# Optimization experiments

Measured on AMD Instinct MI355X. Metric: run time of the kernel, lower is better.

Reference implementation:

```python
import jax, jax.numpy as jnp
import numpy as np
import math

B, T, C, H = 2, 2048, 1024, 16
D = C // H  # head dim 64

def setup_inputs() -> dict:
    key = jax.random.key(0)
    ks = jax.random.split(key, 3)
    scale = 0.02
    return {
        "x": jax.random.normal(ks[0], (B, T, C), dtype=jnp.float32),
        "W_attn": jax.random.normal(ks[1], (C, 3 * C), dtype=jnp.float32) * scale,
        "b_attn": jnp.zeros((3 * C,), dtype=jnp.float32),
        "W_proj": jax.random.normal(ks[2], (C, C), dtype=jnp.float32) * scale,
        "b_proj": jnp.zeros((C,), dtype=jnp.float32),
    }

def reference(x, W_attn, b_attn, W_proj, b_proj):
    Bb, Tt, Cc = x.shape
    qkv = x @ W_attn + b_attn                       # [B,T,3C]
    q, k, v = jnp.split(qkv, 3, axis=-1)
    # [B,T,C] -> [B,H,T,D]
    def heads(t):
        return t.reshape(Bb, Tt, H, D).transpose(0, 2, 1, 3)
    q, k, v = heads(q), heads(k), heads(v)
    scores = jnp.einsum('bhqd,bhkd->bhqk', q, k) * (1.0 / math.sqrt(D))
    causal = jnp.tril(jnp.ones((Tt, Tt), dtype=bool))
    scores = jnp.where(causal, scores, -jnp.inf)
    attn = jax.nn.softmax(scores, axis=-1)
    out = jnp.einsum('bhqk,bhkd->bhqd', attn, v)    # [B,H,T,D]
    out = out.transpose(0, 2, 1, 3).reshape(Bb, Tt, Cc)
    return out @ W_proj + b_proj
```

## Files before the change

### kernel.cpp

```cpp
#include <hip/hip_runtime.h>

typedef unsigned short u16;
typedef unsigned int u32;
typedef float f32x4 __attribute__((ext_vector_type(4)));
typedef float f32x16 __attribute__((ext_vector_type(16)));
typedef unsigned int u32x4 __attribute__((ext_vector_type(4)));
typedef unsigned int u32x2 __attribute__((ext_vector_type(2)));
typedef unsigned short u16x8 __attribute__((ext_vector_type(8)));
typedef unsigned short u16x4 __attribute__((ext_vector_type(4)));

#define DEV static __device__ __forceinline__

constexpr int BB = 2, TT = 2048, CC = 1024, HH = 16, DD = 64;
constexpr int MDIM = BB * TT;

DEV u16 f2bf(float f) {
  unsigned int u = __builtin_bit_cast(unsigned int, f);
  u += 0x7fffu + ((u >> 16) & 1u);
  return (u16)(u >> 16);
}
DEV float bf2f(u16 h) {
  unsigned int u = ((unsigned int)h) << 16;
  return __builtin_bit_cast(float, u);
}
DEV void async16(const void* g, void* l) {
  __builtin_amdgcn_global_load_lds(
      (const __attribute__((address_space(1))) unsigned int*)g,
      (__attribute__((address_space(3))) unsigned int*)l, 16, 0, 0);
}
DEV void mfma16(f32x4& acc, u32x4 a, u32x4 b) {
  asm volatile("v_mfma_f32_16x16x32_bf16 %0, %1, %2, %0"
               : "+v"(acc)
               : "v"(a), "v"(b));
}
DEV void mfma32(f32x16& acc, u32x4 a, u32x4 b) {
  asm volatile("v_mfma_f32_32x32x16_bf16 %0, %1, %2, %0"
               : "+v"(acc)
               : "v"(a), "v"(b));
}
DEV u32 cvtpk(float lo, float hi) {
  u32 r;
  asm("v_cvt_pk_bf16_f32 %0, %1, %2" : "=v"(r) : "v"(lo), "v"(hi));
  return r;
}
DEV void pswap(u32& a, u32& b) {
#if __has_builtin(__builtin_amdgcn_permlane32_swap)
  u32x2 r = __builtin_amdgcn_permlane32_swap(a, b, false, false);
  a = r.x;
  b = r.y;
#else
  asm volatile("v_permlane32_swap_b32 %0, %1" : "+v"(a), "+v"(b));
#endif
}
DEV float exp2g(float x) {
#if __has_builtin(__builtin_amdgcn_exp2f)
  return __builtin_amdgcn_exp2f(x);
#else
  return exp2f(x);
#endif
}

__global__ void cvt_f32_bf16(const float* __restrict__ in, u16* __restrict__ out, int n) {
  const int i = (blockIdx.x * blockDim.x + threadIdx.x) * 4;
  if (i < n) {
    f32x4 v = *(const f32x4*)(in + i);
    u16x4 o;
#pragma unroll
    for (int j = 0; j < 4; ++j) o[j] = f2bf(v[j]);
    *(u16x4*)(out + i) = o;
  }
}

__global__ void transpose_both(const float* __restrict__ Wa, const float* __restrict__ Wp,
                               u16* __restrict__ Wa_t, u16* __restrict__ Wp_t) {
  __shared__ float tile[32][33];
  int bx = blockIdx.x;
  const float* in;
  u16* out;
  int Cc;
  if (bx < 96) { in = Wa; out = Wa_t; Cc = 3072; }
  else { bx -= 96; in = Wp; out = Wp_t; Cc = 1024; }
  const int R = 1024;
  const int x0 = bx * 32, y0 = blockIdx.y * 32;
  const int tx = threadIdx.x, ty = threadIdx.y;
  tile[ty][tx] = in[(size_t)(y0 + ty) * Cc + (x0 + tx)];
  __syncthreads();
  out[(size_t)(x0 + ty) * R + (y0 + tx)] = f2bf(tile[tx][ty]);
}

template <int MODE>
__global__ __launch_bounds__(256) void gemm_bf16(
    const u16* __restrict__ A, const u16* __restrict__ Bt,
    const float* __restrict__ bias, float* __restrict__ outF,
    u16* __restrict__ qw, u16* __restrict__ kw, u16* __restrict__ vw,
    int M, int N, int K) {
  __shared__ alignas(16) u16 Sh[2][128 * 64];
  u16* Asp = Sh[0];
  u16* Bsp = Sh[1];
  const int tid = threadIdx.x;
  const int lane = tid & 63, w = tid >> 6;
  const int g = lane >> 4, c16 = lane & 15;
  const int wm = (w >> 1) * 64, wn = (w & 1) * 64;

  const int wgid = blockIdx.y * gridDim.x + blockIdx.x;
  const int xcd = wgid & 7, pi = wgid >> 3;
  int bxs, bys;
  if (MODE == 1) {
    bxs = 12 * (xcd & 1) + pi % 12;
    bys = 8 * (xcd >> 1) + pi / 12;
  } else {
    bxs = pi & 7;
    bys = 4 * xcd + (pi >> 3);
  }
  const int brow = bys * 128, bcol = bxs * 128;

  const int lrow = lane >> 3;
  const int scol = ((lane & 7) ^ lrow) << 4;
  const int rswz = (c16 & 7) << 4;

  f32x4 acc[4][4];
#pragma unroll
  for (int m = 0; m < 4; ++m)
#pragma unroll
    for (int n = 0; n < 4; ++n) acc[m][n] = f32x4{0.f, 0.f, 0.f, 0.f};

  const size_t ldb = (size_t)K * 2;
  const char* Abase = (const char*)A + (size_t)brow * ldb;
  const char* Bbase = (const char*)Bt + (size_t)bcol * ldb;

  for (int kt = 0; kt < K; kt += 64) {
    __syncthreads();
#pragma unroll
    for (int i = 0; i < 4; ++i) {
      const int chunk = i * 4 + w;
      const int row = chunk * 8 + lrow;
      async16(Abase + (size_t)row * ldb + (size_t)kt * 2 + scol, (char*)Asp + chunk * 1024);
      async16(Bbase + (size_t)row * ldb + (size_t)kt * 2 + scol, (char*)Bsp + chunk * 1024);
    }
    __syncthreads();
#pragma unroll
    for (int kc = 0; kc < 2; ++kc) {
      const int cb = (kc * 64 + g * 16) ^ rswz;
      u32x4 af[4], bf8[4];
#pragma unroll
      for (int m = 0; m < 4; ++m)
        af[m] = *(const u32x4*)((const char*)Asp + (wm + m * 16 + c16) * 128 + cb);
#pragma unroll
      for (int n = 0; n < 4; ++n)
        bf8[n] = *(const u32x4*)((const char*)Bsp + (wn + n * 16 + c16) * 128 + cb);
#pragma unroll
      for (int m = 0; m < 4; ++m)
#pragma unroll
        for (int n = 0; n < 4; ++n) mfma16(acc[m][n], af[m], bf8[n]);
    }
  }

  if (MODE == 0) {
    float* Ef = (float*)&Sh[0][0];
#pragma unroll
    for (int pass = 0; pass < 2; ++pass) {
      __syncthreads();
      if ((wm >> 6) == pass) {
#pragma unroll
        for (int n = 0; n < 4; ++n) {
          const float bv = bias[bcol + wn + n * 16 + c16];
#pragma unroll
          for (int m = 0; m < 4; ++m)
#pragma unroll
            for (int r = 0; r < 4; ++r)
              Ef[(m * 16 + g * 4 + r) * 128 + wn + n * 16 + c16] = acc[m][n][r] + bv;
        }
      }
      __syncthreads();
#pragma unroll
      for (int i = 0; i < 8; ++i) {
        const int chunk = tid + i * 256;
        const int row = chunk >> 5;
        const int c4 = (chunk & 31) * 4;
        f32x4 v4 = *(const f32x4*)&Ef[row * 128 + c4];
        *(f32x4*)&outF[(size_t)(brow + pass * 64 + row) * N + bcol + c4] = v4;
      }
    }
  } else {
    u16* E = &Sh[0][0];
    const int which = bcol >> 10;
    __syncthreads();
    if (which < 2) {
#pragma unroll
      for (int n = 0; n < 4; ++n) {
        const float bv = bias[bcol + wn + n * 16 + c16];
#pragma unroll
        for (int m = 0; m < 4; ++m)
#pragma unroll
          for (int r = 0; r < 4; ++r)
            E[(wm + m * 16 + g * 4 + r) * 128 + wn + n * 16 + c16] =
                f2bf(acc[m][n][r] + bv);
      }
    } else {
#pragma unroll
      for (int n = 0; n < 4; ++n) {
        const float bv = bias[bcol + wn + n * 16 + c16];
#pragma unroll
        for (int m = 0; m < 4; ++m) {
          u16x4 t4;
#pragma unroll
          for (int r = 0; r < 4; ++r) t4[r] = f2bf(acc[m][n][r] + bv);
          *(u16x4*)&E[(wn + n * 16 + c16) * 128 + wm + m * 16 + g * 4] = t4;
        }
      }
    }
    __syncthreads();
#pragma unroll
    for (int i = 0; i < 8; ++i) {
      const int chunk = tid + i * 256;
      if (which < 2) {
        const int row = chunk >> 4;
        const int cc8 = (chunk & 15) * 8;
        const int colg = bcol + cc8;
        const int c = colg & 1023, h = c >> 6, d = c & 63;
        const int rowg = brow + row, b = rowg >> 11, t = rowg & (TT - 1);
        u16x8 v8 = *(const u16x8*)&E[row * 128 + cc8];
        u16* dst = (which == 0 ? qw : kw) + ((size_t)(b * HH + h) * TT + t) * DD + d;
        *(u16x8*)dst = v8;
      } else {
        const int drow = chunk >> 4;
        const int t8 = (chunk & 15) * 8;
        const int colg = bcol + drow;
        const int c = colg & 1023, h = c >> 6, d = c & 63;
        const int rowg = brow + t8, b = rowg >> 11, t = rowg & (TT - 1);
        u16x8 v8 = *(const u16x8*)&E[drow * 128 + t8];
        u16* dst = vw + ((size_t)(b * HH + h) * DD + d) * TT + t;
        *(u16x8*)dst = v8;
      }
    }
  }
}

__global__ __launch_bounds__(256) void attn_fwd(
    const u16* __restrict__ qw, const u16* __restrict__ kw,
    const u16* __restrict__ vw, u16* __restrict__ ao) {
  extern __shared__ u16 smem[];
  const int tid = threadIdx.x;
  const int lane = tid & 63, w = tid >> 6;
  const int ql = lane & 31, half = lane >> 5;
  const int bh = blockIdx.y;
  const int qb = ((bh >> 4) & 1) ? (15 - blockIdx.x) : blockIdx.x;
  const int q0w = qb * 128 + w * 32;
  const int qg = q0w + ql;
  const int lrow = lane >> 3;
  const int scol = ((lane & 7) ^ lrow) << 4;
  const int rswz = (ql & 7) << 4;

  u32x4 qf[4];
  {
    const u16* qrow = qw + ((size_t)bh * TT + qg) * DD;
    const float qs = 0.125f * 1.44269504f;
#pragma unroll
    for (int dwin = 0; dwin < 4; ++dwin) {
      u16x8 u = *(const u16x8*)(qrow + dwin * 16 + half * 8);
      u16x8 s;
#pragma unroll
      for (int j = 0; j < 8; ++j) s[j] = f2bf(bf2f(u[j]) * qs);
      qf[dwin] = __builtin_bit_cast(u32x4, s);
    }
  }

  f32x16 o0, o1;
#pragma unroll
  for (int i = 0; i < 16; ++i) { o0[i] = 0.f; o1[i] = 0.f; }
  float l_run = 0.f;

  const char* kbase = (const char*)kw + ((size_t)bh * TT) * 128;
  const char* vbase = (const char*)vw + ((size_t)bh * DD) * (TT * 2);

  const int nt = 2 * qb + 2;

  auto kptr = [&](int b) { return (char*)(smem + b * 4096); };
  auto vptr = [&](int b) { return (char*)(smem + 16384 + b * 4096); };

  auto STAGE = [&](int kt_) {
    if (kt_ >= nt) return;
    const int buf = kt_ & 3;
    const int t0_ = kt_ * 64;
#pragma unroll
    for (int i_ = 0; i_ < 2; ++i_) {
      const int chunk = w * 2 + i_;
      const int row = chunk * 8 + lrow;
      async16(kbase + (size_t)(t0_ + row) * 128 + scol, kptr(buf) + chunk * 1024);
      async16(vbase + (size_t)row * (TT * 2) + (size_t)t0_ * 2 + scol,
              vptr(buf) + chunk * 1024);
    }
  };

  auto QK = [&](int kt_, f32x16& sa, f32x16& sb) {
    const char* Kc = kptr(kt_ & 3);
#pragma unroll
    for (int i = 0; i < 16; ++i) { sa[i] = 0.f; sb[i] = 0.f; }
    __builtin_amdgcn_s_setprio(1);
#pragma unroll
    for (int dwin = 0; dwin < 4; ++dwin) {
      const int cb = (dwin * 32 + half * 16) ^ rswz;
      u32x4 ak0 = *(const u32x4*)(Kc + (0 + ql) * 128 + cb);
      u32x4 ak1 = *(const u32x4*)(Kc + (32 + ql) * 128 + cb);
      mfma32(sa, ak0, qf[dwin]);
      mfma32(sb, ak1, qf[dwin]);
    }
    __builtin_amdgcn_s_setprio(0);
  };

  auto FINISH = [&](int kt_, f32x16& s0, f32x16& s1) {
    const int t0 = kt_ * 64;
    if (t0 >= q0w + 32) return;
    if (t0 + 63 > q0w) {
      const int kb = t0 + 4 * half - qg;
#pragma unroll
      for (int r = 0; r < 16; ++r) {
        const int ko = (r & 3) + 8 * (r >> 2);
        if (kb + ko > 0) s0[r] = -1e30f;
        if (kb + 32 + ko > 0) s1[r] = -1e30f;
      }
    }
#pragma unroll
    for (int i = 0; i < 16; ++i) {
      s0[i] = exp2g(s0[i]);
      s1[i] = exp2g(s1[i]);
    }
    float a8[8];
#pragma unroll
    for (int i = 0; i < 8; ++i)
      a8[i] = (s0[i] + s0[i + 8]) + (s1[i] + s1[i + 8]);
    float rs = ((a8[0] + a8[1]) + (a8[2] + a8[3])) + ((a8[4] + a8[5]) + (a8[6] + a8[7]));
    rs += __shfl_xor(rs, 32, 64);
    l_run += rs;

    u32x4 pf[4];
#pragma unroll
    for (int win = 0; win < 4; ++win) {
      const int b = (win & 1) * 8;
      u32 w0, w1, w2, w3;
      if (win < 2) {
        w0 = cvtpk(s0[b + 0], s0[b + 1]); w2 = cvtpk(s0[b + 4], s0[b + 5]);
        w1 = cvtpk(s0[b + 2], s0[b + 3]); w3 = cvtpk(s0[b + 6], s0[b + 7]);
      } else {
        w0 = cvtpk(s1[b + 0], s1[b + 1]); w2 = cvtpk(s1[b + 4], s1[b + 5]);
        w1 = cvtpk(s1[b + 2], s1[b + 3]); w3 = cvtpk(s1[b + 6], s1[b + 7]);
      }
      pswap(w0, w2);
      pswap(w1, w3);
      pf[win] = u32x4{w0, w1, w2, w3};
    }
    const char* Vc = vptr(kt_ & 3);
    __builtin_amdgcn_s_setprio(1);
#pragma unroll
    for (int win = 0; win < 4; ++win) {
      const int cb = (win * 32 + half * 16) ^ rswz;
      u32x4 av0 = *(const u32x4*)(Vc + (0 + ql) * 128 + cb);
      u32x4 av1 = *(const u32x4*)(Vc + (32 + ql) * 128 + cb);
      mfma32(o0, av0, pf[win]);
      mfma32(o1, av1, pf[win]);
    }
    __builtin_amdgcn_s_setprio(0);
  };

  STAGE(0);
  STAGE(1);
  STAGE(2);
  if (nt >= 3)
    asm volatile("s_waitcnt vmcnt(8)" ::: "memory");
  else
    asm volatile("s_waitcnt vmcnt(4)" ::: "memory");
  __builtin_amdgcn_sched_barrier(0);
  __builtin_amdgcn_s_barrier();
  __builtin_amdgcn_sched_barrier(0);

  f32x16 sA0, sA1, sB0, sB1;
  QK(0, sA0, sA1);

#define BODY(KT, C0, C1, N0, N1)                                          \
  {                                                                       \
    const int kt_b = (KT);                                                \
    if (kt_b + 2 < nt)                                                    \
      asm volatile("s_waitcnt vmcnt(4)" ::: "memory");                    \
    else                                                                  \
      asm volatile("s_waitcnt vmcnt(0)" ::: "memory");                    \
    __builtin_amdgcn_sched_barrier(0);                                    \
    __builtin_amdgcn_s_barrier();                                         \
    __builtin_amdgcn_sched_barrier(0);                                    \
    STAGE(kt_b + 3);                                                      \
    if (kt_b + 1 < nt && (kt_b + 1) * 64 < q0w + 32) QK(kt_b + 1, N0, N1);\
    FINISH(kt_b, C0, C1);                                                 \
  }

  for (int kt2 = 0; kt2 < nt; kt2 += 2) {
    BODY(kt2, sA0, sA1, sB0, sB1);
    BODY(kt2 + 1, sB0, sB1, sA0, sA1);
  }
#undef BODY

  const int b = bh >> 4, h = bh & 15;
  const float inv = 1.f / l_run;
  u16* aorow = ao + ((size_t)(b * TT) + qg) * CC + h * DD;
#pragma unroll
  for (int rg = 0; rg < 4; ++rg) {
    u16x4 t0v, t1v;
#pragma unroll
    for (int j = 0; j < 4; ++j) {
      t0v[j] = f2bf(o0[rg * 4 + j] * inv);
      t1v[j] = f2bf(o1[rg * 4 + j] * inv);
    }
    *(u16x4*)(aorow + 8 * rg + 4 * half) = t0v;
    *(u16x4*)(aorow + 32 + 8 * rg + 4 * half) = t1v;
  }
}

extern "C" void kernel_launch(void* const* d_in, const int* in_sizes, int n_in,
                              void* d_out, int out_size, void* d_ws, size_t ws_size,
                              hipStream_t stream) {
  const float* x  = (const float*)d_in[0];
  const float* Wa = (const float*)d_in[1];
  const float* ba = (const float*)d_in[2];
  const float* Wp = (const float*)d_in[3];
  const float* bp = (const float*)d_in[4];
  float* out = (float*)d_out;

  char* ws = (char*)d_ws;
  const size_t MB = 1ull << 20;
  u16* x_bf = (u16*)(ws);
  u16* ao   = (u16*)(ws);
  u16* Wa_t = (u16*)(ws + 8 * MB);
  u16* Wp_t = (u16*)(ws + 14 * MB);
  u16* q_ws = (u16*)(ws + 16 * MB);
  u16* k_ws = (u16*)(ws + 24 * MB);
  u16* v_ws = (u16*)(ws + 32 * MB);

  hipLaunchKernelGGL(cvt_f32_bf16, dim3((MDIM * CC) / 1024), dim3(256), 0, stream,
                     x, x_bf, MDIM * CC);
  hipLaunchKernelGGL(transpose_both, dim3(128, 32), dim3(32, 32), 0, stream,
                     Wa, Wp, Wa_t, Wp_t);
  hipLaunchKernelGGL((gemm_bf16<1>), dim3(3 * CC / 128, MDIM / 128), dim3(256), 0, stream,
                     x_bf, Wa_t, ba, nullptr, q_ws, k_ws, v_ws, MDIM, 3 * CC, CC);
  hipLaunchKernelGGL(attn_fwd, dim3(TT / 128, BB * HH), dim3(256), 65536, stream,
                     q_ws, k_ws, v_ws, ao);
  hipLaunchKernelGGL((gemm_bf16<0>), dim3(CC / 128, MDIM / 128), dim3(256), 0, stream,
                     ao, Wp_t, bp, out, nullptr, nullptr, nullptr, MDIM, CC, CC);
}
```

Before: 110.9 us.

## Halve attention KV tile to 32 keys and fuse prep kernels

The attention kernel now processes 32-key tiles instead of 64. This halves the score registers and the shared memory per block, from 64KB to 32KB, with a new swizzle for V rows that are 64 bytes wide. The x conversion and the weight transposes are merged into one prep_all launch to remove a kernel launch. The change trades higher occupancy and less wasted work on the causal diagonal for more barriers and loop iterations per block.

```diff
diff --git a/kernel.cpp b/kernel.cpp
--- a/kernel.cpp
+++ b/kernel.cpp
@@ -60,21 +60,23 @@
 #endif
 }
 
-__global__ void cvt_f32_bf16(const float* __restrict__ in, u16* __restrict__ out, int n) {
-  const int i = (blockIdx.x * blockDim.x + threadIdx.x) * 4;
-  if (i < n) {
-    f32x4 v = *(const f32x4*)(in + i);
-    u16x4 o;
-#pragma unroll
-    for (int j = 0; j < 4; ++j) o[j] = f2bf(v[j]);
-    *(u16x4*)(out + i) = o;
-  }
-}
-
-__global__ void transpose_both(const float* __restrict__ Wa, const float* __restrict__ Wp,
-                               u16* __restrict__ Wa_t, u16* __restrict__ Wp_t) {
+__global__ void prep_all(const float* __restrict__ x,
+                         const float* __restrict__ Wa, const float* __restrict__ Wp,
+                         u16* __restrict__ x_bf,
+                         u16* __restrict__ Wa_t, u16* __restrict__ Wp_t) {
   __shared__ float tile[32][33];
   int bx = blockIdx.x;
+  const int tx = threadIdx.x, ty = threadIdx.y;
+  if (bx >= 128) {
+    const int cb = (bx - 128) * 32 + blockIdx.y;
+    const int i = (cb * 1024 + ty * 32 + tx) * 4;
+    f32x4 v = *(const f32x4*)(x + i);
+    u16x4 o;
+#pragma unroll
+    for (int j = 0; j < 4; ++j) o[j] = f2bf(v[j]);
+    *(u16x4*)(x_bf + i) = o;
+    return;
+  }
   const float* in;
   u16* out;
   int Cc;
@@ -82,7 +84,6 @@
   else { bx -= 96; in = Wp; out = Wp_t; Cc = 1024; }
   const int R = 1024;
   const int x0 = bx * 32, y0 = blockIdx.y * 32;
-  const int tx = threadIdx.x, ty = threadIdx.y;
   tile[ty][tx] = in[(size_t)(y0 + ty) * Cc + (x0 + tx)];
   __syncthreads();
   out[(size_t)(x0 + ty) * R + (y0 + tx)] = f2bf(tile[tx][ty]);
@@ -250,6 +251,8 @@
   const int lrow = lane >> 3;
   const int scol = ((lane & 7) ^ lrow) << 4;
   const int rswz = (ql & 7) << 4;
+  const int vsrc = ((lane & 3) ^ ((lane >> 3) & 3)) << 4;
+  const int vrswz = ((ql >> 1) & 3) << 4;
 
   u32x4 qf[4];
   {
@@ -273,78 +276,63 @@
   const char* kbase = (const char*)kw + ((size_t)bh * TT) * 128;
   const char* vbase = (const char*)vw + ((size_t)bh * DD) * (TT * 2);
 
-  const int nt = 2 * qb + 2;
-
-  auto kptr = [&](int b) { return (char*)(smem + b * 4096); };
-  auto vptr = [&](int b) { return (char*)(smem + 16384 + b * 4096); };
+  const int nt = 4 * (qb + 1);
+
+  auto kptr = [&](int b) { return (char*)smem + b * 4096; };
+  auto vptr = [&](int b) { return (char*)smem + 16384 + b * 4096; };
 
   auto STAGE = [&](int kt_) {
     if (kt_ >= nt) return;
     const int buf = kt_ & 3;
-    const int t0_ = kt_ * 64;
-#pragma unroll
-    for (int i_ = 0; i_ < 2; ++i_) {
-      const int chunk = w * 2 + i_;
-      const int row = chunk * 8 + lrow;
-      async16(kbase + (size_t)(t0_ + row) * 128 + scol, kptr(buf) + chunk * 1024);
-      async16(vbase + (size_t)row * (TT * 2) + (size_t)t0_ * 2 + scol,
-              vptr(buf) + chunk * 1024);
-    }
+    const int t0_ = kt_ * 32;
+    const int krow = w * 8 + lrow;
+    async16(kbase + (size_t)(t0_ + krow) * 128 + scol, kptr(buf) + w * 1024);
+    const int vrow = w * 16 + (lane >> 2);
+    async16(vbase + (size_t)vrow * (TT * 2) + (size_t)t0_ * 2 + vsrc,
+            vptr(buf) + w * 1024);
   };
 
-  auto QK = [&](int kt_, f32x16& sa, f32x16& sb) {
+  auto QK = [&](int kt_, f32x16& sa) {
     const char* Kc = kptr(kt_ & 3);
 #pragma unroll
-    for (int i = 0; i < 16; ++i) { sa[i] = 0.f; sb[i] = 0.f; }
+    for (int i = 0; i < 16; ++i) sa[i] = 0.f;
     __builtin_amdgcn_s_setprio(1);
 #pragma unroll
     for (int dwin = 0; dwin < 4; ++dwin) {
       const int cb = (dwin * 32 + half * 16) ^ rswz;
-      u32x4 ak0 = *(const u32x4*)(Kc + (0 + ql) * 128 + cb);
-      u32x4 ak1 = *(const u32x4*)(Kc + (32 + ql) * 128 + cb);
-      mfma32(sa, ak0, qf[dwin]);
-      mfma32(sb, ak1, qf[dwin]);
+      u32x4 ak = *(const u32x4*)(Kc + ql * 128 + cb);
+      mfma32(sa, ak, qf[dwin]);
     }
     __builtin_amdgcn_s_setprio(0);
   };
 
-  auto FINISH = [&](int kt_, f32x16& s0, f32x16& s1) {
-    const int t0 = kt_ * 64;
+  auto FINISH = [&](int kt_, f32x16& s) {
+    const int t0 = kt_ * 32;
     if (t0 >= q0w + 32) return;
-    if (t0 + 63 > q0w) {
+    if (t0 + 31 > q0w) {
       const int kb = t0 + 4 * half - qg;
 #pragma unroll
       for (int r = 0; r < 16; ++r) {
         const int ko = (r & 3) + 8 * (r >> 2);
-        if (kb + ko > 0) s0[r] = -1e30f;
-        if (kb + 32 + ko > 0) s1[r] = -1e30f;
-      }
-    }
-#pragma unroll
-    for (int i = 0; i < 16; ++i) {
-      s0[i] = exp2g(s0[i]);
-      s1[i] = exp2g(s1[i]);
-    }
-    float a8[8];
-#pragma unroll
-    for (int i = 0; i < 8; ++i)
-      a8[i] = (s0[i] + s0[i + 8]) + (s1[i] + s1[i + 8]);
-    float rs = ((a8[0] + a8[1]) + (a8[2] + a8[3])) + ((a8[4] + a8[5]) + (a8[6] + a8[7]));
+        if (kb + ko > 0) s[r] = -1e30f;
+      }
+    }
+#pragma unroll
+    for (int i = 0; i < 16; ++i) s[i] = exp2g(s[i]);
+    float a4[4];
+#pragma unroll
+    for (int i = 0; i < 4; ++i)
+      a4[i] = (s[i] + s[i + 4]) + (s[i + 8] + s[i + 12]);
+    float rs = (a4[0] + a4[1]) + (a4[2] + a4[3]);
     rs += __shfl_xor(rs, 32, 64);
     l_run += rs;
 
-    u32x4 pf[4];
-#pragma unroll
-    for (int win = 0; win < 4; ++win) {
-      const int b = (win & 1) * 8;
-      u32 w0, w1, w2, w3;
-      if (win < 2) {
-        w0 = cvtpk(s0[b + 0], s0[b + 1]); w2 = cvtpk(s0[b + 4], s0[b + 5]);
-        w1 = cvtpk(s0[b + 2], s0[b + 3]); w3 = cvtpk(s0[b + 6], s0[b + 7]);
-      } else {
-        w0 = cvtpk(s1[b + 0], s1[b + 1]); w2 = cvtpk(s1[b + 4], s1[b + 5]);
-        w1 = cvtpk(s1[b + 2], s1[b + 3]); w3 = cvtpk(s1[b + 6], s1[b + 7]);
-      }
+    u32x4 pf[2];
+#pragma unroll
+    for (int win = 0; win < 2; ++win) {
+      const int b = win * 8;
+      u32 w0 = cvtpk(s[b + 0], s[b + 1]), w2 = cvtpk(s[b + 4], s[b + 5]);
+      u32 w1 = cvtpk(s[b + 2], s[b + 3]), w3 = cvtpk(s[b + 6], s[b + 7]);
       pswap(w0, w2);
       pswap(w1, w3);
       pf[win] = u32x4{w0, w1, w2, w3};
@@ -352,10 +340,10 @@
     const char* Vc = vptr(kt_ & 3);
     __builtin_amdgcn_s_setprio(1);
 #pragma unroll
-    for (int win = 0; win < 4; ++win) {
-      const int cb = (win * 32 + half * 16) ^ rswz;
-      u32x4 av0 = *(const u32x4*)(Vc + (0 + ql) * 128 + cb);
-      u32x4 av1 = *(const u32x4*)(Vc + (32 + ql) * 128 + cb);
+    for (int win = 0; win < 2; ++win) {
+      const int cb = (win * 32 + half * 16) ^ vrswz;
+      u32x4 av0 = *(const u32x4*)(Vc + (0 + ql) * 64 + cb);
+      u32x4 av1 = *(const u32x4*)(Vc + (32 + ql) * 64 + cb);
       mfma32(o0, av0, pf[win]);
       mfma32(o1, av1, pf[win]);
     }
@@ -365,35 +353,32 @@
   STAGE(0);
   STAGE(1);
   STAGE(2);
-  if (nt >= 3)
-    asm volatile("s_waitcnt vmcnt(8)" ::: "memory");
-  else
-    asm volatile("s_waitcnt vmcnt(4)" ::: "memory");
+  asm volatile("s_waitcnt vmcnt(4)" ::: "memory");
   __builtin_amdgcn_sched_barrier(0);
   __builtin_amdgcn_s_barrier();
   __builtin_amdgcn_sched_barrier(0);
 
-  f32x16 sA0, sA1, sB0, sB1;
-  QK(0, sA0, sA1);
-
-#define BODY(KT, C0, C1, N0, N1)                                          \
+  f32x16 sA, sB;
+  QK(0, sA);
+
+#define BODY(KT, C, N)                                                    \
   {                                                                       \
     const int kt_b = (KT);                                                \
     if (kt_b + 2 < nt)                                                    \
-      asm volatile("s_waitcnt vmcnt(4)" ::: "memory");                    \
+      asm volatile("s_waitcnt vmcnt(2)" ::: "memory");                    \
     else                                                                  \
       asm volatile("s_waitcnt vmcnt(0)" ::: "memory");                    \
     __builtin_amdgcn_sched_barrier(0);                                    \
     __builtin_amdgcn_s_barrier();                                         \
     __builtin_amdgcn_sched_barrier(0);                                    \
     STAGE(kt_b + 3);                                                      \
-    if (kt_b + 1 < nt && (kt_b + 1) * 64 < q0w + 32) QK(kt_b + 1, N0, N1);\
-    FINISH(kt_b, C0, C1);                                                 \
+    if (kt_b + 1 < nt && (kt_b + 1) * 32 < q0w + 32) QK(kt_b + 1, N);     \
+    FINISH(kt_b, C);                                                      \
   }
 
   for (int kt2 = 0; kt2 < nt; kt2 += 2) {
-    BODY(kt2, sA0, sA1, sB0, sB1);
-    BODY(kt2 + 1, sB0, sB1, sA0, sA1);
+    BODY(kt2, sA, sB);
+    BODY(kt2 + 1, sB, sA);
   }
 #undef BODY
 
@@ -433,13 +418,11 @@
   u16* k_ws = (u16*)(ws + 24 * MB);
   u16* v_ws = (u16*)(ws + 32 * MB);
 
-  hipLaunchKernelGGL(cvt_f32_bf16, dim3((MDIM * CC) / 1024), dim3(256), 0, stream,
-                     x, x_bf, MDIM * CC);
-  hipLaunchKernelGGL(transpose_both, dim3(128, 32), dim3(32, 32), 0, stream,
-                     Wa, Wp, Wa_t, Wp_t);
+  hipLaunchKernelGGL(prep_all, dim3(160, 32), dim3(32, 32), 0, stream,
+                     x, Wa, Wp, x_bf, Wa_t, Wp_t);
   hipLaunchKernelGGL((gemm_bf16<1>), dim3(3 * CC / 128, MDIM / 128), dim3(256), 0, stream,
                      x_bf, Wa_t, ba, nullptr, q_ws, k_ws, v_ws, MDIM, 3 * CC, CC);
-  hipLaunchKernelGGL(attn_fwd, dim3(TT / 128, BB * HH), dim3(256), 65536, stream,
+  hipLaunchKernelGGL(attn_fwd, dim3(TT / 128, BB * HH), dim3(256), 32768, stream,
                      q_ws, k_ws, v_ws, ao);
   hipLaunchKernelGGL((gemm_bf16<0>), dim3(CC / 128, MDIM / 128), dim3(256), 0, stream,
                      ao, Wp_t, bp, out, nullptr, nullptr, nullptr, MDIM, CC, CC);
```

After: 117.4 us. +5.9%, slower.

## Split KV range for long causal query blocks and merge prep kernels

Applied to the files above, without the earlier changes.

The causal attention kernel now launches 24 blocks per head instead of 16. The 8 short query tiles run whole, and each of the 8 long tiles is split into two halves over the key range, which balances work across blocks. Each half writes an unnormalized bf16 partial output and its row sum, and a new combine kernel adds the halves and normalizes them. Separately, the x conversion and the weight transposes are merged into a single prep kernel to save one launch. In exchange this adds a combine launch, extra global traffic for the partial results, and some rounding from storing unnormalized partials in bf16.

```diff
diff --git a/kernel.cpp b/kernel.cpp
--- a/kernel.cpp
+++ b/kernel.cpp
@@ -60,21 +60,23 @@
 #endif
 }
 
-__global__ void cvt_f32_bf16(const float* __restrict__ in, u16* __restrict__ out, int n) {
-  const int i = (blockIdx.x * blockDim.x + threadIdx.x) * 4;
-  if (i < n) {
-    f32x4 v = *(const f32x4*)(in + i);
-    u16x4 o;
-#pragma unroll
-    for (int j = 0; j < 4; ++j) o[j] = f2bf(v[j]);
-    *(u16x4*)(out + i) = o;
-  }
-}
-
-__global__ void transpose_both(const float* __restrict__ Wa, const float* __restrict__ Wp,
-                               u16* __restrict__ Wa_t, u16* __restrict__ Wp_t) {
+__global__ void prep_all(const float* __restrict__ x,
+                         const float* __restrict__ Wa, const float* __restrict__ Wp,
+                         u16* __restrict__ x_bf,
+                         u16* __restrict__ Wa_t, u16* __restrict__ Wp_t) {
   __shared__ float tile[32][33];
   int bx = blockIdx.x;
+  const int tx = threadIdx.x, ty = threadIdx.y;
+  if (bx >= 128) {
+    const int cb = (bx - 128) * 32 + blockIdx.y;
+    const int i = (cb * 1024 + ty * 32 + tx) * 4;
+    f32x4 v = *(const f32x4*)(x + i);
+    u16x4 o;
+#pragma unroll
+    for (int j = 0; j < 4; ++j) o[j] = f2bf(v[j]);
+    *(u16x4*)(x_bf + i) = o;
+    return;
+  }
   const float* in;
   u16* out;
   int Cc;
@@ -82,7 +84,6 @@
   else { bx -= 96; in = Wp; out = Wp_t; Cc = 1024; }
   const int R = 1024;
   const int x0 = bx * 32, y0 = blockIdx.y * 32;
-  const int tx = threadIdx.x, ty = threadIdx.y;
   tile[ty][tx] = in[(size_t)(y0 + ty) * Cc + (x0 + tx)];
   __syncthreads();
   out[(size_t)(x0 + ty) * R + (y0 + tx)] = f2bf(tile[tx][ty]);
@@ -238,13 +239,24 @@
 
 __global__ __launch_bounds__(256) void attn_fwd(
     const u16* __restrict__ qw, const u16* __restrict__ kw,
-    const u16* __restrict__ vw, u16* __restrict__ ao) {
+    const u16* __restrict__ vw, u16* __restrict__ ao,
+    u16* __restrict__ O1, float* __restrict__ lpart) {
   extern __shared__ u16 smem[];
   const int tid = threadIdx.x;
   const int lane = tid & 63, w = tid >> 6;
   const int ql = lane & 31, half = lane >> 5;
   const int bh = blockIdx.y;
-  const int qb = ((bh >> 4) & 1) ? (15 - blockIdx.x) : blockIdx.x;
+  int bx = blockIdx.x;
+  if (bh & 1) bx = 23 - bx;
+  int qb, t_begin, cnt, sp;
+  if (bx < 8) {
+    qb = bx; sp = -1; t_begin = 0; cnt = 2 * qb + 2;
+  } else {
+    const int i = bx - 8;
+    qb = 8 + (i >> 1); sp = i & 1; cnt = qb + 1; t_begin = sp * cnt;
+  }
+  const int t_end = t_begin + cnt;
+
   const int q0w = qb * 128 + w * 32;
   const int qg = q0w + ql;
   const int lrow = lane >> 3;
@@ -273,27 +285,24 @@
   const char* kbase = (const char*)kw + ((size_t)bh * TT) * 128;
   const char* vbase = (const char*)vw + ((size_t)bh * DD) * (TT * 2);
 
-  const int nt = 2 * qb + 2;
-
-  auto kptr = [&](int b) { return (char*)(smem + b * 4096); };
-  auto vptr = [&](int b) { return (char*)(smem + 16384 + b * 4096); };
+  auto kptr = [&](int b) { return (char*)(smem + (b & 3) * 4096); };
+  auto vptr = [&](int b) { return (char*)(smem + 16384 + (b & 3) * 4096); };
 
   auto STAGE = [&](int kt_) {
-    if (kt_ >= nt) return;
-    const int buf = kt_ & 3;
+    if (kt_ >= t_end) return;
     const int t0_ = kt_ * 64;
 #pragma unroll
     for (int i_ = 0; i_ < 2; ++i_) {
       const int chunk = w * 2 + i_;
       const int row = chunk * 8 + lrow;
-      async16(kbase + (size_t)(t0_ + row) * 128 + scol, kptr(buf) + chunk * 1024);
+      async16(kbase + (size_t)(t0_ + row) * 128 + scol, kptr(kt_) + chunk * 1024);
       async16(vbase + (size_t)row * (TT * 2) + (size_t)t0_ * 2 + scol,
-              vptr(buf) + chunk * 1024);
+              vptr(kt_) + chunk * 1024);
     }
   };
 
   auto QK = [&](int kt_, f32x16& sa, f32x16& sb) {
-    const char* Kc = kptr(kt_ & 3);
+    const char* Kc = kptr(kt_);
 #pragma unroll
     for (int i = 0; i < 16; ++i) { sa[i] = 0.f; sb[i] = 0.f; }
     __builtin_amdgcn_s_setprio(1);
@@ -349,7 +358,7 @@
       pswap(w1, w3);
       pf[win] = u32x4{w0, w1, w2, w3};
     }
-    const char* Vc = vptr(kt_ & 3);
+    const char* Vc = vptr(kt_);
     __builtin_amdgcn_s_setprio(1);
 #pragma unroll
     for (int win = 0; win < 4; ++win) {
@@ -362,10 +371,10 @@
     __builtin_amdgcn_s_setprio(0);
   };
 
-  STAGE(0);
-  STAGE(1);
-  STAGE(2);
-  if (nt >= 3)
+  STAGE(t_begin);
+  if (cnt > 1) STAGE(t_begin + 1);
+  if (cnt > 2) STAGE(t_begin + 2);
+  if (cnt >= 3)
     asm volatile("s_waitcnt vmcnt(8)" ::: "memory");
   else
     asm volatile("s_waitcnt vmcnt(4)" ::: "memory");
@@ -374,12 +383,12 @@
   __builtin_amdgcn_sched_barrier(0);
 
   f32x16 sA0, sA1, sB0, sB1;
-  QK(0, sA0, sA1);
+  QK(t_begin, sA0, sA1);
 
 #define BODY(KT, C0, C1, N0, N1)                                          \
   {                                                                       \
     const int kt_b = (KT);                                                \
-    if (kt_b + 2 < nt)                                                    \
+    if (kt_b + 2 < t_end)                                                 \
       asm volatile("s_waitcnt vmcnt(4)" ::: "memory");                    \
     else                                                                  \
       asm volatile("s_waitcnt vmcnt(0)" ::: "memory");                    \
@@ -387,30 +396,72 @@
     __builtin_amdgcn_s_barrier();                                         \
     __builtin_amdgcn_sched_barrier(0);                                    \
     STAGE(kt_b + 3);                                                      \
-    if (kt_b + 1 < nt && (kt_b + 1) * 64 < q0w + 32) QK(kt_b + 1, N0, N1);\
+    if (kt_b + 1 < t_end && (kt_b + 1) * 64 < q0w + 32) QK(kt_b + 1, N0, N1);\
     FINISH(kt_b, C0, C1);                                                 \
   }
 
-  for (int kt2 = 0; kt2 < nt; kt2 += 2) {
-    BODY(kt2, sA0, sA1, sB0, sB1);
-    BODY(kt2 + 1, sB0, sB1, sA0, sA1);
-  }
+  int j = 0;
+  for (; j + 1 < cnt; j += 2) {
+    BODY(t_begin + j, sA0, sA1, sB0, sB1);
+    BODY(t_begin + j + 1, sB0, sB1, sA0, sA1);
+  }
+  if (j < cnt) BODY(t_begin + j, sA0, sA1, sB0, sB1);
 #undef BODY
 
   const int b = bh >> 4, h = bh & 15;
-  const float inv = 1.f / l_run;
-  u16* aorow = ao + ((size_t)(b * TT) + qg) * CC + h * DD;
-#pragma unroll
-  for (int rg = 0; rg < 4; ++rg) {
-    u16x4 t0v, t1v;
-#pragma unroll
-    for (int j = 0; j < 4; ++j) {
-      t0v[j] = f2bf(o0[rg * 4 + j] * inv);
-      t1v[j] = f2bf(o1[rg * 4 + j] * inv);
-    }
-    *(u16x4*)(aorow + 8 * rg + 4 * half) = t0v;
-    *(u16x4*)(aorow + 32 + 8 * rg + 4 * half) = t1v;
-  }
+  if (sp < 0) {
+    const float inv = 1.f / l_run;
+    u16* aorow = ao + ((size_t)(b * TT) + qg) * CC + h * DD;
+#pragma unroll
+    for (int rg = 0; rg < 4; ++rg) {
+      u16x4 t0v, t1v;
+#pragma unroll
+      for (int jj = 0; jj < 4; ++jj) {
+        t0v[jj] = f2bf(o0[rg * 4 + jj] * inv);
+        t1v[jj] = f2bf(o1[rg * 4 + jj] * inv);
+      }
+      *(u16x4*)(aorow + 8 * rg + 4 * half) = t0v;
+      *(u16x4*)(aorow + 32 + 8 * rg + 4 * half) = t1v;
+    }
+  } else {
+    u16* dst;
+    int stride;
+    if (sp == 0) { dst = ao + ((size_t)(b * TT) + qg) * CC + h * DD; stride = 1; }
+    else { dst = O1 + ((size_t)bh * 1024 + (qg - 1024)) * DD; stride = 1; }
+    (void)stride;
+#pragma unroll
+    for (int rg = 0; rg < 4; ++rg) {
+      u16x4 t0v, t1v;
+#pragma unroll
+      for (int jj = 0; jj < 4; ++jj) {
+        t0v[jj] = f2bf(o0[rg * 4 + jj]);
+        t1v[jj] = f2bf(o1[rg * 4 + jj]);
+      }
+      *(u16x4*)(dst + 8 * rg + 4 * half) = t0v;
+      *(u16x4*)(dst + 32 + 8 * rg + 4 * half) = t1v;
+    }
+    if (half == 0) lpart[(size_t)sp * 32768 + bh * 1024 + (qg - 1024)] = l_run;
+  }
+}
+
+__global__ __launch_bounds__(256) void combine(
+    const u16* __restrict__ O1, const float* __restrict__ lpart,
+    u16* __restrict__ ao) {
+  const int gid = blockIdx.x * 256 + threadIdx.x;
+  const int d8 = gid & 7;
+  const int qq = (gid >> 3) & 1023;
+  const int bh = gid >> 13;
+  const int b = bh >> 4, h = bh & 15;
+  const float l = lpart[bh * 1024 + qq] + lpart[32768 + bh * 1024 + qq];
+  const float inv = 1.f / l;
+  u16* pa = ao + ((size_t)(b * TT + 1024 + qq)) * CC + h * DD + d8 * 8;
+  const u16* p1 = O1 + ((size_t)bh * 1024 + qq) * DD + d8 * 8;
+  u16x8 a = *(const u16x8*)pa;
+  u16x8 c = *(const u16x8*)p1;
+  u16x8 o;
+#pragma unroll
+  for (int jj = 0; jj < 8; ++jj) o[jj] = f2bf((bf2f(a[jj]) + bf2f(c[jj])) * inv);
+  *(u16x8*)pa = o;
 }
 
 extern "C" void kernel_launch(void* const* d_in, const int* in_sizes, int n_in,
@@ -428,19 +479,20 @@
   u16* x_bf = (u16*)(ws);
   u16* ao   = (u16*)(ws);
   u16* Wa_t = (u16*)(ws + 8 * MB);
+  u16* O1   = (u16*)(ws + 8 * MB);
+  float* lp = (float*)(ws + 12 * MB);
   u16* Wp_t = (u16*)(ws + 14 * MB);
   u16* q_ws = (u16*)(ws + 16 * MB);
   u16* k_ws = (u16*)(ws + 24 * MB);
   u16* v_ws = (u16*)(ws + 32 * MB);
 
-  hipLaunchKernelGGL(cvt_f32_bf16, dim3((MDIM * CC) / 1024), dim3(256), 0, stream,
-                     x, x_bf, MDIM * CC);
-  hipLaunchKernelGGL(transpose_both, dim3(128, 32), dim3(32, 32), 0, stream,
-                     Wa, Wp, Wa_t, Wp_t);
+  hipLaunchKernelGGL(prep_all, dim3(160, 32), dim3(32, 32), 0, stream,
+                     x, Wa, Wp, x_bf, Wa_t, Wp_t);
   hipLaunchKernelGGL((gemm_bf16<1>), dim3(3 * CC / 128, MDIM / 128), dim3(256), 0, stream,
                      x_bf, Wa_t, ba, nullptr, q_ws, k_ws, v_ws, MDIM, 3 * CC, CC);
-  hipLaunchKernelGGL(attn_fwd, dim3(TT / 128, BB * HH), dim3(256), 65536, stream,
-                     q_ws, k_ws, v_ws, ao);
+  hipLaunchKernelGGL(attn_fwd, dim3(24, BB * HH), dim3(256), 65536, stream,
+                     q_ws, k_ws, v_ws, ao, O1, lp);
+  hipLaunchKernelGGL(combine, dim3(1024), dim3(256), 0, stream, O1, lp, ao);
   hipLaunchKernelGGL((gemm_bf16<0>), dim3(CC / 128, MDIM / 128), dim3(256), 0, stream,
                      ao, Wp_t, bp, out, nullptr, nullptr, nullptr, MDIM, CC, CC);
 }
```

Result: slower. 117.2 us (+5.7%).

## Use 256x256 pipelined QKV GEMM tile and fuse prep kernels

Applied to the files above, without the earlier changes.

Replaces the 128x128 QKV projection GEMM with a 512-thread kernel that computes 256x256 tiles. It uses 128KB of dynamic LDS for a double-buffered, async-staged K pipeline with explicit waitcnt and barriers, a new swizzle and an XCD-aware block mapping, aiming for more operand reuse and fewer blocks. It also merges the x conversion and the weight transposes into one prep kernel to save a launch. The cost is very high LDS use per block, which limits occupancy, plus fragile hand-written synchronisation.

```diff
diff --git a/kernel.cpp b/kernel.cpp
--- a/kernel.cpp
+++ b/kernel.cpp
@@ -60,21 +60,23 @@
 #endif
 }
 
-__global__ void cvt_f32_bf16(const float* __restrict__ in, u16* __restrict__ out, int n) {
-  const int i = (blockIdx.x * blockDim.x + threadIdx.x) * 4;
-  if (i < n) {
-    f32x4 v = *(const f32x4*)(in + i);
-    u16x4 o;
-#pragma unroll
-    for (int j = 0; j < 4; ++j) o[j] = f2bf(v[j]);
-    *(u16x4*)(out + i) = o;
-  }
-}
-
-__global__ void transpose_both(const float* __restrict__ Wa, const float* __restrict__ Wp,
-                               u16* __restrict__ Wa_t, u16* __restrict__ Wp_t) {
+__global__ void prep_all(const float* __restrict__ x,
+                         const float* __restrict__ Wa, const float* __restrict__ Wp,
+                         u16* __restrict__ x_bf,
+                         u16* __restrict__ Wa_t, u16* __restrict__ Wp_t) {
   __shared__ float tile[32][33];
   int bx = blockIdx.x;
+  const int tx = threadIdx.x, ty = threadIdx.y;
+  if (bx >= 128) {
+    const int cb = (bx - 128) * 32 + blockIdx.y;
+    const int i = (cb * 1024 + ty * 32 + tx) * 4;
+    f32x4 v = *(const f32x4*)(x + i);
+    u16x4 o;
+#pragma unroll
+    for (int j = 0; j < 4; ++j) o[j] = f2bf(v[j]);
+    *(u16x4*)(x_bf + i) = o;
+    return;
+  }
   const float* in;
   u16* out;
   int Cc;
@@ -82,17 +84,146 @@
   else { bx -= 96; in = Wp; out = Wp_t; Cc = 1024; }
   const int R = 1024;
   const int x0 = bx * 32, y0 = blockIdx.y * 32;
-  const int tx = threadIdx.x, ty = threadIdx.y;
   tile[ty][tx] = in[(size_t)(y0 + ty) * Cc + (x0 + tx)];
   __syncthreads();
   out[(size_t)(x0 + ty) * R + (y0 + tx)] = f2bf(tile[tx][ty]);
 }
 
-template <int MODE>
-__global__ __launch_bounds__(256) void gemm_bf16(
+__global__ __launch_bounds__(512, 2) void gemm_qkv256(
+    const u16* __restrict__ A, const u16* __restrict__ Bt,
+    const float* __restrict__ bias,
+    u16* __restrict__ qw, u16* __restrict__ kw, u16* __restrict__ vw) {
+  extern __shared__ char smem[];
+  const int K = CC, NT = K / 64;
+  const int tid = threadIdx.x;
+  const int lane = tid & 63, w = tid >> 6;
+  const int g = lane >> 4, c16 = lane & 15;
+  const int wm2 = (w >> 2) * 128, wn2 = (w & 3) * 64;
+
+  const int wgid = blockIdx.x;
+  const int xcd = wgid & 7, idx = wgid >> 3;
+  const int bxs = (xcd & 3) * 3 + idx % 3;
+  const int bys = (xcd >> 2) * 8 + idx / 3;
+  const int brow = bys * 256, bcol = bxs * 256;
+
+  const int ssw = ((lane & 3) ^ ((lane >> 3) & 3)) << 4;
+  const int rsw = (g ^ ((c16 >> 1) & 3)) << 4;
+
+  f32x4 acc[8][4];
+#pragma unroll
+  for (int m = 0; m < 8; ++m)
+#pragma unroll
+    for (int n = 0; n < 4; ++n) acc[m][n] = f32x4{0.f, 0.f, 0.f, 0.f};
+
+  const size_t ldb = (size_t)K * 2;
+  const char* Abase = (const char*)A + (size_t)brow * ldb;
+  const char* Bbase = (const char*)Bt + (size_t)bcol * ldb;
+
+  auto STAGE = [&](int kt, int kh) {
+    const int par = kt & 1;
+    char* Adst = smem + (par * 2 + kh) * 16384;
+    char* Bdst = smem + 65536 + (par * 2 + kh) * 16384;
+    const size_t koff = (size_t)kt * 128 + kh * 64;
+#pragma unroll
+    for (int i = 0; i < 2; ++i) {
+      const int c = w * 2 + i;
+      const int row = c * 16 + (lane >> 2);
+      async16(Abase + (size_t)row * ldb + koff + ssw, Adst + c * 1024);
+      async16(Bbase + (size_t)row * ldb + koff + ssw, Bdst + c * 1024);
+    }
+  };
+
+  STAGE(0, 0); STAGE(0, 1);
+  STAGE(1, 0); STAGE(1, 1);
+
+  for (int kt = 0; kt < NT; ++kt) {
+    const int par = kt & 1;
+    if (kt + 1 < NT)
+      asm volatile("s_waitcnt vmcnt(8)" ::: "memory");
+    else
+      asm volatile("s_waitcnt vmcnt(0)" ::: "memory");
+    __builtin_amdgcn_sched_barrier(0);
+    __builtin_amdgcn_s_barrier();
+    __builtin_amdgcn_sched_barrier(0);
+#pragma unroll
+    for (int kc = 0; kc < 2; ++kc) {
+      const char* Ap = smem + (par * 2 + kc) * 16384;
+      const char* Bp = smem + 65536 + (par * 2 + kc) * 16384;
+      u32x4 af[8], bf[4];
+#pragma unroll
+      for (int m = 0; m < 8; ++m)
+        af[m] = *(const u32x4*)(Ap + (wm2 + m * 16 + c16) * 64 + rsw);
+#pragma unroll
+      for (int n = 0; n < 4; ++n)
+        bf[n] = *(const u32x4*)(Bp + (wn2 + n * 16 + c16) * 64 + rsw);
+      asm volatile("s_waitcnt lgkmcnt(0)" ::: "memory");
+      __builtin_amdgcn_sched_barrier(0);
+      __builtin_amdgcn_s_setprio(1);
+#pragma unroll
+      for (int m = 0; m < 8; ++m)
+#pragma unroll
+        for (int n = 0; n < 4; ++n) mfma16(acc[m][n], af[m], bf[n]);
+      __builtin_amdgcn_s_setprio(0);
+      __builtin_amdgcn_s_barrier();
+      if (kt + 2 < NT) STAGE(kt + 2, kc);
+    }
+  }
+
+  u16* E = (u16*)smem;
+  const int which = bcol >> 10;
+  if (which < 2) {
+#pragma unroll
+    for (int n = 0; n < 4; ++n) {
+      const float bv = bias[bcol + wn2 + n * 16 + c16];
+#pragma unroll
+      for (int m = 0; m < 8; ++m)
+#pragma unroll
+        for (int r = 0; r < 4; ++r)
+          E[(wm2 + m * 16 + g * 4 + r) * 256 + wn2 + n * 16 + c16] =
+              f2bf(acc[m][n][r] + bv);
+    }
+  } else {
+#pragma unroll
+    for (int n = 0; n < 4; ++n) {
+      const float bv = bias[bcol + wn2 + n * 16 + c16];
+#pragma unroll
+      for (int m = 0; m < 8; ++m) {
+        u16x4 t4;
+#pragma unroll
+        for (int r = 0; r < 4; ++r) t4[r] = f2bf(acc[m][n][r] + bv);
+        *(u16x4*)&E[(wn2 + n * 16 + c16) * 256 + wm2 + m * 16 + g * 4] = t4;
+      }
+    }
+  }
+  __syncthreads();
+#pragma unroll
+  for (int i = 0; i < 16; ++i) {
+    const int chunk = tid + i * 512;
+    if (which < 2) {
+      const int row = chunk >> 5;
+      const int col8 = (chunk & 31) * 8;
+      const int colg = bcol + col8;
+      const int c = colg & 1023, h = c >> 6, d = c & 63;
+      const int rowg = brow + row, b = rowg >> 11, t = rowg & (TT - 1);
+      u16x8 v8 = *(const u16x8*)&E[row * 256 + col8];
+      u16* dst = (which == 0 ? qw : kw) + ((size_t)(b * HH + h) * TT + t) * DD + d;
+      *(u16x8*)dst = v8;
+    } else {
+      const int drow = chunk >> 5;
+      const int t8 = (chunk & 31) * 8;
+      const int colg = bcol + drow;
+      const int c = colg & 1023, h = c >> 6, d = c & 63;
+      const int rowg = brow + t8, b = rowg >> 11, t = rowg & (TT - 1);
+      u16x8 v8 = *(const u16x8*)&E[drow * 256 + t8];
+      u16* dst = vw + ((size_t)(b * HH + h) * DD + d) * TT + t;
+      *(u16x8*)dst = v8;
+    }
+  }
+}
+
+__global__ __launch_bounds__(256) void gemm_proj(
     const u16* __restrict__ A, const u16* __restrict__ Bt,
     const float* __restrict__ bias, float* __restrict__ outF,
-    u16* __restrict__ qw, u16* __restrict__ kw, u16* __restrict__ vw,
     int M, int N, int K) {
   __shared__ alignas(16) u16 Sh[2][128 * 64];
   u16* Asp = Sh[0];
@@ -104,14 +235,8 @@
 
   const int wgid = blockIdx.y * gridDim.x + blockIdx.x;
   const int xcd = wgid & 7, pi = wgid >> 3;
-  int bxs, bys;
-  if (MODE == 1) {
-    bxs = 12 * (xcd & 1) + pi % 12;
-    bys = 8 * (xcd >> 1) + pi / 12;
-  } else {
-    bxs = pi & 7;
-    bys = 4 * xcd + (pi >> 3);
-  }
+  const int bxs = pi & 7;
+  const int bys = 4 * xcd + (pi >> 3);
   const int brow = bys * 128, bcol = bxs * 128;
 
   const int lrow = lane >> 3;
@@ -155,37 +280,11 @@
     }
   }
 
-  if (MODE == 0) {
-    float* Ef = (float*)&Sh[0][0];
-#pragma unroll
-    for (int pass = 0; pass < 2; ++pass) {
-      __syncthreads();
-      if ((wm >> 6) == pass) {
-#pragma unroll
-        for (int n = 0; n < 4; ++n) {
-          const float bv = bias[bcol + wn + n * 16 + c16];
-#pragma unroll
-          for (int m = 0; m < 4; ++m)
-#pragma unroll
-            for (int r = 0; r < 4; ++r)
-              Ef[(m * 16 + g * 4 + r) * 128 + wn + n * 16 + c16] = acc[m][n][r] + bv;
-        }
-      }
-      __syncthreads();
-#pragma unroll
-      for (int i = 0; i < 8; ++i) {
-        const int chunk = tid + i * 256;
-        const int row = chunk >> 5;
-        const int c4 = (chunk & 31) * 4;
-        f32x4 v4 = *(const f32x4*)&Ef[row * 128 + c4];
-        *(f32x4*)&outF[(size_t)(brow + pass * 64 + row) * N + bcol + c4] = v4;
-      }
-    }
-  } else {
-    u16* E = &Sh[0][0];
-    const int which = bcol >> 10;
+  float* Ef = (float*)&Sh[0][0];
+#pragma unroll
+  for (int pass = 0; pass < 2; ++pass) {
     __syncthreads();
-    if (which < 2) {
+    if ((wm >> 6) == pass) {
 #pragma unroll
       for (int n = 0; n < 4; ++n) {
         const float bv = bias[bcol + wn + n * 16 + c16];
@@ -193,45 +292,17 @@
         for (int m = 0; m < 4; ++m)
 #pragma unroll
           for (int r = 0; r < 4; ++r)
-            E[(wm + m * 16 + g * 4 + r) * 128 + wn + n * 16 + c16] =
-                f2bf(acc[m][n][r] + bv);
-      }
-    } else {
-#pragma unroll
-      for (int n = 0; n < 4; ++n) {
-        const float bv = bias[bcol + wn + n * 16 + c16];
-#pragma unroll
-        for (int m = 0; m < 4; ++m) {
-          u16x4 t4;
-#pragma unroll
-          for (int r = 0; r < 4; ++r) t4[r] = f2bf(acc[m][n][r] + bv);
-          *(u16x4*)&E[(wn + n * 16 + c16) * 128 + wm + m * 16 + g * 4] = t4;
-        }
+            Ef[(m * 16 + g * 4 + r) * 128 + wn + n * 16 + c16] = acc[m][n][r] + bv;
       }
     }
     __syncthreads();
 #pragma unroll
     for (int i = 0; i < 8; ++i) {
       const int chunk = tid + i * 256;
-      if (which < 2) {
-        const int row = chunk >> 4;
-        const int cc8 = (chunk & 15) * 8;
-        const int colg = bcol + cc8;
-        const int c = colg & 1023, h = c >> 6, d = c & 63;
-        const int rowg = brow + row, b = rowg >> 11, t = rowg & (TT - 1);
-        u16x8 v8 = *(const u16x8*)&E[row * 128 + cc8];
-        u16* dst = (which == 0 ? qw : kw) + ((size_t)(b * HH + h) * TT + t) * DD + d;
-        *(u16x8*)dst = v8;
-      } else {
-        const int drow = chunk >> 4;
-        const int t8 = (chunk & 15) * 8;
-        const int colg = bcol + drow;
-        const int c = colg & 1023, h = c >> 6, d = c & 63;
-        const int rowg = brow + t8, b = rowg >> 11, t = rowg & (TT - 1);
-        u16x8 v8 = *(const u16x8*)&E[drow * 128 + t8];
-        u16* dst = vw + ((size_t)(b * HH + h) * DD + d) * TT + t;
-        *(u16x8*)dst = v8;
-      }
+      const int row = chunk >> 5;
+      const int c4 = (chunk & 31) * 4;
+      f32x4 v4 = *(const f32x4*)&Ef[row * 128 + c4];
+      *(f32x4*)&outF[(size_t)(brow + pass * 64 + row) * N + bcol + c4] = v4;
     }
   }
 }
@@ -239,7 +310,7 @@
 __global__ __launch_bounds__(256) void attn_fwd(
     const u16* __restrict__ qw, const u16* __restrict__ kw,
     const u16* __restrict__ vw, u16* __restrict__ ao) {
-  extern __shared__ u16 smem[];
+  extern __shared__ u16 smem_a[];
   const int tid = threadIdx.x;
   const int lane = tid & 63, w = tid >> 6;
   const int ql = lane & 31, half = lane >> 5;
@@ -275,25 +346,24 @@
 
   const int nt = 2 * qb + 2;
 
-  auto kptr = [&](int b) { return (char*)(smem + b * 4096); };
-  auto vptr = [&](int b) { return (char*)(smem + 16384 + b * 4096); };
+  auto kptr = [&](int b) { return (char*)(smem_a + (b & 3) * 4096); };
+  auto vptr = [&](int b) { return (char*)(smem_a + 16384 + (b & 3) * 4096); };
 
   auto STAGE = [&](int kt_) {
     if (kt_ >= nt) return;
-    const int buf = kt_ & 3;
     const int t0_ = kt_ * 64;
 #pragma unroll
     for (int i_ = 0; i_ < 2; ++i_) {
       const int chunk = w * 2 + i_;
       const int row = chunk * 8 + lrow;
-      async16(kbase + (size_t)(t0_ + row) * 128 + scol, kptr(buf) + chunk * 1024);
+      async16(kbase + (size_t)(t0_ + row) * 128 + scol, kptr(kt_) + chunk * 1024);
       async16(vbase + (size_t)row * (TT * 2) + (size_t)t0_ * 2 + scol,
-              vptr(buf) + chunk * 1024);
+              vptr(kt_) + chunk * 1024);
     }
   };
 
   auto QK = [&](int kt_, f32x16& sa, f32x16& sb) {
-    const char* Kc = kptr(kt_ & 3);
+    const char* Kc = kptr(kt_);
 #pragma unroll
     for (int i = 0; i < 16; ++i) { sa[i] = 0.f; sb[i] = 0.f; }
     __builtin_amdgcn_s_setprio(1);
@@ -349,7 +419,7 @@
       pswap(w1, w3);
       pf[win] = u32x4{w0, w1, w2, w3};
     }
-    const char* Vc = vptr(kt_ & 3);
+    const char* Vc = vptr(kt_);
     __builtin_amdgcn_s_setprio(1);
 #pragma unroll
     for (int win = 0; win < 4; ++win) {
@@ -433,14 +503,21 @@
   u16* k_ws = (u16*)(ws + 24 * MB);
   u16* v_ws = (u16*)(ws + 32 * MB);
 
-  hipLaunchKernelGGL(cvt_f32_bf16, dim3((MDIM * CC) / 1024), dim3(256), 0, stream,
-                     x, x_bf, MDIM * CC);
-  hipLaunchKernelGGL(transpose_both, dim3(128, 32), dim3(32, 32), 0, stream,
-                     Wa, Wp, Wa_t, Wp_t);
-  hipLaunchKernelGGL((gemm_bf16<1>), dim3(3 * CC / 128, MDIM / 128), dim3(256), 0, stream,
-                     x_bf, Wa_t, ba, nullptr, q_ws, k_ws, v_ws, MDIM, 3 * CC, CC);
+  static bool attr_set = []() {
+    hipFuncSetAttribute((const void*)gemm_qkv256,
+                        hipFuncAttributeMaxDynamicSharedMemorySize, 131072);
+    hipFuncSetAttribute((const void*)attn_fwd,
+                        hipFuncAttributeMaxDynamicSharedMemorySize, 65536);
+    return true;
+  }();
+  (void)attr_set;
+
+  hipLaunchKernelGGL(prep_all, dim3(160, 32), dim3(32, 32), 0, stream,
+                     x, Wa, Wp, x_bf, Wa_t, Wp_t);
+  hipLaunchKernelGGL(gemm_qkv256, dim3(192), dim3(512), 131072, stream,
+                     x_bf, Wa_t, ba, q_ws, k_ws, v_ws);
   hipLaunchKernelGGL(attn_fwd, dim3(TT / 128, BB * HH), dim3(256), 65536, stream,
                      q_ws, k_ws, v_ws, ao);
-  hipLaunchKernelGGL((gemm_bf16<0>), dim3(CC / 128, MDIM / 128), dim3(256), 0, stream,
-                     ao, Wp_t, bp, out, nullptr, nullptr, nullptr, MDIM, CC, CC);
-}
+  hipLaunchKernelGGL(gemm_proj, dim3(CC / 128, MDIM / 128), dim3(256), 0, stream,
+                     ao, Wp_t, bp, out, MDIM, CC, CC);
+}
```

Result: no change. 110.7 us (-0.2%).
